# Kernel optimization log

Hardware: AMD Instinct MI355X
Metric: run time of the kernel (lower is better)

The kernel has to match this reference:

```python
import jax, jax.numpy as jnp
from jax import lax
import numpy as np

# Model hyper-parameters (from init_kwargs)
B = 4
POINT_NUM = 32768
SKP_NUM = 512
ISK_NUM = 2
K1 = 32                       # skp_neighbor_num
K2 = int(K1 * SKP_NUM * 4 / POINT_NUM)   # = 2, as computed in __init__
RADIUS_SCALING = 1.5
SPHERE_N = 128                # points per sphere template


def _fibonacci_sphere(n):
    i = np.arange(n, dtype=np.float64) + 0.5
    phi = np.arccos(1.0 - 2.0 * i / n)
    theta = np.pi * (1.0 + 5.0 ** 0.5) * i
    return np.stack([np.cos(theta) * np.sin(phi),
                     np.sin(theta) * np.sin(phi),
                     np.cos(phi)], axis=-1).astype(np.float32)


def setup_inputs() -> dict:
    key = jax.random.key(0)
    xyz = jax.random.normal(key, (B, POINT_NUM, 3), dtype=jnp.float32)
    sphere_template = jnp.asarray(_fibonacci_sphere(SPHERE_N))  # [S,3] unit sphere
    return {"xyz": xyz, "sphere_template": sphere_template}


def _fps(xyz, n):
    """Iterative furthest point sampling. xyz: [B,N,3] -> indices [B,n] int32."""
    b, N, _ = xyz.shape
    dist0 = jnp.full((b, N), 1e10, dtype=xyz.dtype)
    last0 = jnp.zeros((b,), dtype=jnp.int32)

    def step(carry, _):
        dist, last = carry
        lp = jnp.take_along_axis(xyz, last[:, None, None], axis=1)  # [B,1,3]
        d = jnp.sum((xyz - lp) ** 2, axis=-1)                        # [B,N]
        dist = jnp.minimum(dist, d)
        nxt = jnp.argmax(dist, axis=-1).astype(jnp.int32)
        return (dist, nxt), last

    (_, _), idxs = lax.scan(step, (dist0, last0), None, length=n)
    return idxs.T  # [B,n]


def _pairwise_sqdist(centers, pts):
    # [B,M,N] squared distances
    c2 = jnp.sum(centers ** 2, axis=-1)[:, :, None]
    p2 = jnp.sum(pts ** 2, axis=-1)[:, None, :]
    cp = jnp.einsum('bmd,bnd->bmn', centers, pts)
    return c2 + p2 - 2.0 * cp


def _sklnz(centers, pts, k):
    """SkeletonizationBlock: move each center to the mean of its k nearest
    points in pts; radius = mean distance to those neighbors."""
    d2 = _pairwise_sqdist(centers, pts)          # [B,M,N]
    neg, idx = lax.top_k(-d2, k)                 # [B,M,k]
    nb = jax.vmap(lambda x, i: x[i])(pts, idx)   # [B,M,k,3]
    new_centers = jnp.mean(nb, axis=2)
    radius = jnp.mean(jnp.sqrt(jnp.clip(-neg, 0.0)), axis=2)  # [B,M]
    return new_centers, radius


def _forward(xyz, sphere_template):
    # Stage 1: FPS to 4*skp_num seeds, then iterative skeletonization
    ids = _fps(xyz, SKP_NUM * 4)                               # [B,4*skp]
    centers = jnp.take_along_axis(xyz, ids[:, :, None], axis=1)
    radius = None
    for _ in range(ISK_NUM):
        centers, radius = _sklnz(centers, xyz, K1)
    # Stage 2: FPS on intermediate skeleton down to skp_num
    xyz2 = centers
    ids2 = _fps(xyz2, SKP_NUM)                                 # [B,skp]
    centers = jnp.take_along_axis(xyz2, ids2[:, :, None], axis=1)
    radius = jnp.take_along_axis(radius, ids2, axis=1)
    for _ in range(ISK_NUM):
        centers, _radius = _sklnz(centers, xyz2, K2)
    radius = (radius + _radius) * RADIUS_SCALING               # [B,skp]
    # Sphere reconstruction: template scaled by radius, translated to centers
    sphere_points = centers[:, :, None, :] + radius[:, :, None, None] * sphere_template[None, None]
    return centers, sphere_points, radius


def reference(xyz, sphere_template):
    return _forward(xyz, sphere_template)
```

## Files before the change

kernel.cpp:

```cpp
#include <hip/hip_runtime.h>
#include <cstdint>

#define BATCH 4
#define NPTS  32768
#define QN    8192
#define SKP   512
#define M1    (SKP*4)
#define KA    32
#define KB    2
#define SPHN  128

__device__ __forceinline__ float sqdist(float px, float py, float pz,
                                        float cx, float cy, float cz) {
  float dx = px - cx, dy = py - cy, dz = pz - cz;
  return __fadd_rn(__fadd_rn(__fmul_rn(dx, dx), __fmul_rn(dy, dy)),
                   __fmul_rn(dz, dz));
}
__device__ __forceinline__ float d2gram(float px, float py, float pz,
                                        float qx, float qy, float qz, float q2) {
  float p2 = __fadd_rn(__fadd_rn(__fmul_rn(px, px), __fmul_rn(py, py)),
                       __fmul_rn(pz, pz));
  float cp = __fadd_rn(__fadd_rn(__fmul_rn(qx, px), __fmul_rn(qy, py)),
                       __fmul_rn(qz, pz));
  return __fsub_rn(__fadd_rn(q2, p2), __fadd_rn(cp, cp));
}

__device__ __forceinline__ unsigned long long shfl_xor_u64(unsigned long long v, int off) {
  int lo = __shfl_xor((int)(unsigned)v, off);
  int hi = __shfl_xor((int)(unsigned)(v >> 32), off);
  return ((unsigned long long)(unsigned)hi << 32) | (unsigned)lo;
}
__device__ __forceinline__ unsigned long long shfl_u64(unsigned long long v, int src) {
  int lo = __shfl((int)(unsigned)v, src);
  int hi = __shfl((int)(unsigned)(v >> 32), src);
  return ((unsigned long long)(unsigned)hi << 32) | (unsigned)lo;
}
__device__ __forceinline__ unsigned long long umax64(unsigned long long a, unsigned long long b) {
  return a > b ? a : b;
}
__device__ __forceinline__ unsigned long long umin64(unsigned long long a, unsigned long long b) {
  return a < b ? a : b;
}
__device__ __forceinline__ void ins3(unsigned long long& k1, unsigned long long& k2,
                                     unsigned long long& k3, unsigned long long v) {
  k3 = umax64(k3, umin64(k2, v));
  k2 = umax64(k2, umin64(k1, v));
  k1 = umax64(k1, v);
}
__device__ __forceinline__ void ins4(unsigned long long& k1, unsigned long long& k2,
                                     unsigned long long& k3, unsigned long long& k4,
                                     unsigned long long v) {
  k4 = umax64(k4, umin64(k3, v));
  k3 = umax64(k3, umin64(k2, v));
  k2 = umax64(k2, umin64(k1, v));
  k1 = umax64(k1, v);
}

__global__ __launch_bounds__(1024)
void fps1_kernel(const float* __restrict__ xyz, float4* __restrict__ cen4a,
                 unsigned long long* __restrict__ sync)
{
  int blk = blockIdx.x;
  int b = blk >> 2, sub = blk & 3;
  const float* X = xyz + (size_t)b * NPTS * 3;
  cen4a += (size_t)b * M1;
  int tid = threadIdx.x, lane = tid & 63, wave = tid >> 6;
  int base = sub * QN;

  __shared__ float2 xysh[QN];
  __shared__ unsigned long long s_w[16][4];
  __shared__ float s_pivc[48][3];
  __shared__ int s_J;

  float zr[8], dist[8];
#pragma unroll
  for (int j = 0; j < 8; ++j) {
    int pl = tid + 1024 * j;
    int pg = base + pl;
    xysh[pl] = make_float2(X[3*pg], X[3*pg+1]);
    zr[j] = X[3*pg+2];
    dist[j] = 1e10f;
  }
  if (tid == 0) {
    s_pivc[0][0] = X[0]; s_pivc[0][1] = X[1]; s_pivc[0][2] = X[2];
    if (sub == 0) cen4a[0] = make_float4(X[0], X[1], X[2], 0.f);
  }
  __syncthreads();

  int it = 1, J = 1, rc = 1;

  while (it < M1) {
    for (int jp0 = 0; jp0 < J; jp0 += 4) {
      float pxa[4], pya[4], pza[4];
#pragma unroll
      for (int l = 0; l < 4; ++l) {
        int jj = jp0 + l; jj = (jj < J) ? jj : jp0;
        pxa[l] = s_pivc[jj][0]; pya[l] = s_pivc[jj][1]; pza[l] = s_pivc[jj][2];
      }
#pragma unroll
      for (int j = 0; j < 8; ++j) {
        int pl = tid + 1024 * j;
        float2 c2 = xysh[pl];
        float dd = dist[j];
#pragma unroll
        for (int l = 0; l < 4; ++l)
          dd = fminf(dd, sqdist(c2.x, c2.y, zr[j], pxa[l], pya[l], pza[l]));
        dist[j] = dd;
      }
    }
    unsigned long long k1 = 0, k2 = 0, k3 = 0, k4 = 0;
#pragma unroll
    for (int j = 0; j < 8; ++j) {
      int pg = base + tid + 1024 * j;
      unsigned long long key =
          ((unsigned long long)__float_as_uint(dist[j]) << 15) |
          (unsigned)(0x7FFF - pg);
      ins4(k1, k2, k3, k4, key);
    }
#pragma unroll
    for (int off = 32; off > 0; off >>= 1) {
      unsigned long long o1 = shfl_xor_u64(k1, off);
      unsigned long long o2 = shfl_xor_u64(k2, off);
      unsigned long long o3 = shfl_xor_u64(k3, off);
      unsigned long long o4 = shfl_xor_u64(k4, off);
      ins4(k1, k2, k3, k4, o1);
      ins4(k1, k2, k3, k4, o2);
      ins4(k1, k2, k3, k4, o3);
      ins4(k1, k2, k3, k4, o4);
    }
    if (lane == 0) {
      s_w[wave][0] = k1; s_w[wave][1] = k2; s_w[wave][2] = k3; s_w[wave][3] = k4;
    }
    __syncthreads();
    if (wave == 0) {
      unsigned long long fb = (lane < 16) ? s_w[lane][3] : 0;
#pragma unroll
      for (int off = 8; off > 0; off >>= 1) {
        unsigned long long o = shfl_xor_u64(fb, off);
        if (o > fb) fb = o;
      }
      fb = shfl_u64(fb, 0);
      unsigned tag = (unsigned)rc;
      int par = rc & 1;
      int sbase = ((b * 2 + par) * 4 + sub) * 56;
      if (lane < 48)
        __hip_atomic_store(&sync[sbase + lane],
                           (s_w[lane & 15][lane >> 4] << 12) | tag,
                           __ATOMIC_RELAXED, __HIP_MEMORY_SCOPE_AGENT);
      if (lane == 48)
        __hip_atomic_store(&sync[sbase + 48], (fb << 12) | tag,
                           __ATOMIC_RELAXED, __HIP_MEMORY_SCOPE_AGENT);
      unsigned long long ck[3];
      int slots[3]; bool need[3];
#pragma unroll
      for (int k = 0; k < 3; ++k) {
        int q = lane + 64 * k;
        int r = q / 48, s = q % 48;
        if (r == 0) { ck[k] = s_w[s & 15][s >> 4]; need[k] = false; slots[k] = 0; }
        else {
          slots[k] = ((b * 2 + par) * 4 + ((sub + r) & 3)) * 56 + s;
          need[k] = true; ck[k] = 0;
        }
      }
      bool needf = (lane < 3);
      int fslot = ((b * 2 + par) * 4 + ((sub + 1 + lane) & 3)) * 56 + 48;
      unsigned long long flr = 0;
      while (__any(need[0] || need[1] || need[2] || needf)) {
#pragma unroll
        for (int k = 0; k < 3; ++k) if (need[k]) {
          unsigned long long v = __hip_atomic_load(&sync[slots[k]],
                                  __ATOMIC_RELAXED, __HIP_MEMORY_SCOPE_AGENT);
          if ((unsigned)(v & 0xFFFu) == tag) { ck[k] = v >> 12; need[k] = false; }
        }
        if (needf) {
          unsigned long long v = __hip_atomic_load(&sync[fslot],
                                  __ATOMIC_RELAXED, __HIP_MEMORY_SCOPE_AGENT);
          if ((unsigned)(v & 0xFFFu) == tag) { flr = v >> 12; needf = false; }
        }
      }
      unsigned long long f = fb;
      f = umax64(f, shfl_u64(flr, 0));
      f = umax64(f, shfl_u64(flr, 1));
      f = umax64(f, shfl_u64(flr, 2));
      float cxx[3], cyy[3], czz[3];
#pragma unroll
      for (int k = 0; k < 3; ++k) {
        int ci = 0x7FFF - (int)(ck[k] & 0x7FFFu);
        cxx[k] = X[3*ci]; cyy[k] = X[3*ci+1]; czz[k] = X[3*ci+2];
      }
      int Jn = 0;
      while (it + Jn < M1 && Jn < 48) {
        unsigned long long mk = umax64(umax64(ck[0], ck[1]), ck[2]);
#pragma unroll
        for (int off = 32; off > 0; off >>= 1) {
          unsigned long long o = shfl_xor_u64(mk, off);
          if (o > mk) mk = o;
        }
        if (!(mk > f)) break;
        float px = 0.f, py = 0.f, pz = 0.f;
#pragma unroll
        for (int k = 0; k < 3; ++k) {
          unsigned long long bb = __ballot(ck[k] == mk);
          if (bb) {
            int wl = __ffsll((long long)bb) - 1;
            px = __shfl(cxx[k], wl); py = __shfl(cyy[k], wl); pz = __shfl(czz[k], wl);
            break;
          }
        }
        if (lane == 0) {
          s_pivc[Jn][0] = px; s_pivc[Jn][1] = py; s_pivc[Jn][2] = pz;
          if (sub == 0) cen4a[it + Jn] = make_float4(px, py, pz, 0.f);
        }
#pragma unroll
        for (int k = 0; k < 3; ++k) {
          float d = sqdist(cxx[k], cyy[k], czz[k], px, py, pz);
          float nv = fminf(__uint_as_float((unsigned)(ck[k] >> 15)), d);
          ck[k] = ((unsigned long long)__float_as_uint(nv) << 15) | (ck[k] & 0x7FFFu);
        }
        ++Jn;
      }
      if (lane == 0) s_J = Jn;
    }
    __syncthreads();
    J = s_J;
    it += J;
    rc += 1;
  }
}

__global__ __launch_bounds__(1024)
void fps2_kernel(const float4* __restrict__ pts, int* __restrict__ ids)
{
  int b = blockIdx.x;
  pts += (size_t)b * M1;
  ids += (size_t)b * SKP;
  int tid = threadIdx.x, lane = tid & 63, wave = tid >> 6;

  __shared__ float4 pl[M1];
  __shared__ unsigned long long s_w[16][3];
  __shared__ float s_pivc[16][3];
  __shared__ int s_J;

  float4 f0 = pts[tid], f1 = pts[tid + 1024];
  pl[tid] = f0; pl[tid + 1024] = f1;
  float dist0 = 1e10f, dist1 = 1e10f;
  if (tid == 0) {
    ids[0] = 0;
    s_pivc[0][0] = f0.x; s_pivc[0][1] = f0.y; s_pivc[0][2] = f0.z;
  }
  __syncthreads();

  int it = 1, J = 1;

  while (it < SKP) {
    for (int jp0 = 0; jp0 < J; jp0 += 4) {
      float pxa[4], pya[4], pza[4];
#pragma unroll
      for (int l = 0; l < 4; ++l) {
        int jj = jp0 + l; jj = (jj < J) ? jj : jp0;
        pxa[l] = s_pivc[jj][0]; pya[l] = s_pivc[jj][1]; pza[l] = s_pivc[jj][2];
      }
#pragma unroll
      for (int l = 0; l < 4; ++l) {
        dist0 = fminf(dist0, sqdist(f0.x, f0.y, f0.z, pxa[l], pya[l], pza[l]));
        dist1 = fminf(dist1, sqdist(f1.x, f1.y, f1.z, pxa[l], pya[l], pza[l]));
      }
    }
    unsigned long long k1, k2 = 0, k3 = 0;
    k1 = ((unsigned long long)__float_as_uint(dist0) << 15) | (unsigned)(0x7FFF - tid);
    {
      unsigned long long key =
          ((unsigned long long)__float_as_uint(dist1) << 15) | (unsigned)(0x7FFF - (tid + 1024));
      ins3(k1, k2, k3, key);
    }
#pragma unroll
    for (int off = 32; off > 0; off >>= 1) {
      unsigned long long o1 = shfl_xor_u64(k1, off);
      unsigned long long o2 = shfl_xor_u64(k2, off);
      unsigned long long o3 = shfl_xor_u64(k3, off);
      ins3(k1, k2, k3, o1);
      ins3(k1, k2, k3, o2);
      ins3(k1, k2, k3, o3);
    }
    if (lane == 0) { s_w[wave][0] = k1; s_w[wave][1] = k2; s_w[wave][2] = k3; }
    __syncthreads();
    if (wave == 0) {
      unsigned long long fb = (lane < 16) ? s_w[lane][2] : 0;
#pragma unroll
      for (int off = 8; off > 0; off >>= 1) {
        unsigned long long o = shfl_xor_u64(fb, off);
        if (o > fb) fb = o;
      }
      unsigned long long f = shfl_u64(fb, 0);
      unsigned long long ck = 0;
      if (lane < 16)      ck = s_w[lane][0];
      else if (lane < 32) ck = s_w[lane - 16][1];
      int ci = (0x7FFF - (int)(ck & 0x7FFFu)) & (M1 - 1);
      float4 c = pl[ci];
      int Jn = 0;
      while (it + Jn < SKP && Jn < 16) {
        unsigned long long mk = ck;
#pragma unroll
        for (int off = 32; off > 0; off >>= 1) {
          unsigned long long o = shfl_xor_u64(mk, off);
          if (o > mk) mk = o;
        }
        if (!(mk > f)) break;
        unsigned long long ball = __ballot(ck == mk);
        int wl = __ffsll((long long)ball) - 1;
        float px = __shfl(c.x, wl), py = __shfl(c.y, wl), pz = __shfl(c.z, wl);
        if (lane == 0) {
          s_pivc[Jn][0] = px; s_pivc[Jn][1] = py; s_pivc[Jn][2] = pz;
          ids[it + Jn] = 0x7FFF - (int)(mk & 0x7FFFu);
        }
        float d = sqdist(c.x, c.y, c.z, px, py, pz);
        float nv = fminf(__uint_as_float((unsigned)(ck >> 15)), d);
        ck = ((unsigned long long)__float_as_uint(nv) << 15) | (ck & 0x7FFFu);
        ++Jn;
      }
      if (lane == 0) s_J = Jn;
    }
    __syncthreads();
    J = s_J;
    it += J;
  }
}

template<int K, int KL, int N, bool S3>
__global__ __launch_bounds__(256)
void sklnz_kernel(const float4* __restrict__ queries,
                  const void*   __restrict__ ptsv,
                  float4* __restrict__ outc,
                  float*  __restrict__ outr,
                  int M)
{
  const int CH = N / 64;
  const int CHP = N / 256;
  int wave = threadIdx.x >> 6, lane = threadIdx.x & 63;
  int qid = blockIdx.x * 4 + wave;
  int b = qid / M;
  const float*  P3 = (const float*)ptsv + (size_t)b * N * 3;
  const float4* P4 = (const float4*)ptsv + (size_t)b * N;
  const float4* P4p = (const float4*)P3;
  float4 q = queries[qid];
  float q2 = __fadd_rn(__fadd_rn(__fmul_rn(q.x, q.x), __fmul_rn(q.y, q.y)),
                       __fmul_rn(q.z, q.z));

  __shared__ float heads[4][64][K + 1];

  float a[KL];
#pragma unroll
  for (int s = 0; s < KL; ++s) a[s] = 3.0e38f;
  if constexpr (S3) {
    for (int j = 0; j < CHP; ++j) {
      int u = lane + 64 * j;
      float4 A = P4p[3*u], B = P4p[3*u+1], C = P4p[3*u+2];
      float ds[4];
      ds[0] = d2gram(A.x, A.y, A.z, q.x, q.y, q.z, q2);
      ds[1] = d2gram(A.w, B.x, B.y, q.x, q.y, q.z, q2);
      ds[2] = d2gram(B.z, B.w, C.x, q.x, q.y, q.z, q2);
      ds[3] = d2gram(C.y, C.z, C.w, q.x, q.y, q.z, q2);
#pragma unroll
      for (int e = 0; e < 4; ++e) {
#pragma unroll
        for (int s = KL - 1; s > 0; --s) a[s] = fminf(a[s], fmaxf(a[s-1], ds[e]));
        a[0] = fminf(a[0], ds[e]);
      }
    }
  } else {
    for (int j = 0; j < CH; ++j) {
      float4 f = P4[lane + 64 * j];
      float d = d2gram(f.x, f.y, f.z, q.x, q.y, q.z, q2);
#pragma unroll
      for (int s = KL - 1; s > 0; --s) a[s] = fminf(a[s], fmaxf(a[s-1], d));
      a[0] = fminf(a[0], d);
    }
  }
#pragma unroll
  for (int s = 0; s < KL; ++s) heads[wave][lane][s] = a[s];
  heads[wave][lane][KL] = 3.1e38f;
  int h = 0; float t = 0.f;
  for (int r = 0; r < K; ++r) {
    float mv = heads[wave][lane][h];
    int   ml = lane;
#pragma unroll
    for (int off = 32; off > 0; off >>= 1) {
      float ov = __shfl_xor(mv, off);
      int   ol = __shfl_xor(ml, off);
      if (ov < mv || (ov == mv && ol < ml)) { mv = ov; ml = ol; }
    }
    t = mv;
    if (ml == lane) h++;
  }

  float sx = 0.f, sy = 0.f, sz = 0.f, sr = 0.f;
  int cl = 0;
  int myNext = 0x7fffffff;
  if constexpr (S3) {
    for (int j = 0; j < CHP; ++j) {
      int u = lane + 64 * j;
      float4 A = P4p[3*u], B = P4p[3*u+1], C = P4p[3*u+2];
      float pxs[4] = {A.x, A.w, B.z, C.y};
      float pys[4] = {A.y, B.x, B.w, C.z};
      float pzs[4] = {A.z, B.y, C.x, C.w};
#pragma unroll
      for (int e = 0; e < 4; ++e) {
        float d = d2gram(pxs[e], pys[e], pzs[e], q.x, q.y, q.z, q2);
        if (d < t) { sx += pxs[e]; sy += pys[e]; sz += pzs[e];
                     sr += sqrtf(fmaxf(d, 0.f)); cl++; }
        else if (d == t && myNext == 0x7fffffff) myNext = 4*u + e;
      }
    }
  } else {
    for (int j = 0; j < CH; ++j) {
      int p = lane + 64 * j;
      float4 f = P4[p];
      float d = d2gram(f.x, f.y, f.z, q.x, q.y, q.z, q2);
      if (d < t) { sx += f.x; sy += f.y; sz += f.z; sr += sqrtf(fmaxf(d, 0.f)); cl++; }
      else if (d == t && myNext == 0x7fffffff) myNext = p;
    }
  }
  int ctot = cl;
#pragma unroll
  for (int off = 32; off > 0; off >>= 1) ctot += __shfl_xor(ctot, off);

  if constexpr (KL < K) {
    if (ctot >= K) {
      float a2[K];
#pragma unroll
      for (int s = 0; s < K; ++s) a2[s] = 3.0e38f;
      for (int j = 0; j < CHP; ++j) {
        int u = lane + 64 * j;
        float4 A = P4p[3*u], B = P4p[3*u+1], C = P4p[3*u+2];
        float ds[4];
        ds[0] = d2gram(A.x, A.y, A.z, q.x, q.y, q.z, q2);
        ds[1] = d2gram(A.w, B.x, B.y, q.x, q.y, q.z, q2);
        ds[2] = d2gram(B.z, B.w, C.x, q.x, q.y, q.z, q2);
        ds[3] = d2gram(C.y, C.z, C.w, q.x, q.y, q.z, q2);
#pragma unroll
        for (int e = 0; e < 4; ++e) {
#pragma unroll
          for (int s = K - 1; s > 0; --s) a2[s] = fminf(a2[s], fmaxf(a2[s-1], ds[e]));
          a2[0] = fminf(a2[0], ds[e]);
        }
      }
#pragma unroll
      for (int s = 0; s < K; ++s) heads[wave][lane][s] = a2[s];
      heads[wave][lane][K] = 3.1e38f;
      h = 0;
      for (int r = 0; r < K; ++r) {
        float mv = heads[wave][lane][h];
        int   ml = lane;
#pragma unroll
        for (int off = 32; off > 0; off >>= 1) {
          float ov = __shfl_xor(mv, off);
          int   ol = __shfl_xor(ml, off);
          if (ov < mv || (ov == mv && ol < ml)) { mv = ov; ml = ol; }
        }
        t = mv;
        if (ml == lane) h++;
      }
      sx = sy = sz = sr = 0.f; cl = 0; myNext = 0x7fffffff;
      for (int j = 0; j < CHP; ++j) {
        int u = lane + 64 * j;
        float4 A = P4p[3*u], B = P4p[3*u+1], C = P4p[3*u+2];
        float pxs[4] = {A.x, A.w, B.z, C.y};
        float pys[4] = {A.y, B.x, B.w, C.z};
        float pzs[4] = {A.z, B.y, C.x, C.w};
#pragma unroll
        for (int e = 0; e < 4; ++e) {
          float d = d2gram(pxs[e], pys[e], pzs[e], q.x, q.y, q.z, q2);
          if (d < t) { sx += pxs[e]; sy += pys[e]; sz += pzs[e];
                       sr += sqrtf(fmaxf(d, 0.f)); cl++; }
          else if (d == t && myNext == 0x7fffffff) myNext = 4*u + e;
        }
      }
      ctot = cl;
#pragma unroll
      for (int off = 32; off > 0; off >>= 1) ctot += __shfl_xor(ctot, off);
    }
  }

  int need = K - ctot;
  float rt = sqrtf(fmaxf(t, 0.f));

  for (int e0 = 0; e0 < need; ++e0) {
    int mn = myNext;
#pragma unroll
    for (int off = 32; off > 0; off >>= 1) mn = min(mn, __shfl_xor(mn, off));
    if (myNext == mn) {
      float px, py, pz;
      if (S3) { px = P3[3*mn]; py = P3[3*mn+1]; pz = P3[3*mn+2]; }
      else    { float4 f = P4[mn]; px = f.x; py = f.y; pz = f.z; }
      sx += px; sy += py; sz += pz; sr += rt;
      int nx = 0x7fffffff;
      if constexpr (S3) {
        for (int j = ((mn >> 2) - lane) / 64; j < CHP && nx == 0x7fffffff; ++j) {
          int u = lane + 64 * j;
          float4 A = P4p[3*u], B = P4p[3*u+1], C = P4p[3*u+2];
          float pxs[4] = {A.x, A.w, B.z, C.y};
          float pys[4] = {A.y, B.x, B.w, C.z};
          float pzs[4] = {A.z, B.y, C.x, C.w};
#pragma unroll
          for (int e = 0; e < 4; ++e) {
            int p = 4*u + e;
            float d = d2gram(pxs[e], pys[e], pzs[e], q.x, q.y, q.z, q2);
            if (p > mn && d == t && nx == 0x7fffffff) nx = p;
          }
        }
      } else {
        for (int j = (mn - lane) / 64 + 1; j < CH && nx == 0x7fffffff; ++j) {
          int p = lane + 64 * j;
          float4 f = P4[p];
          float d = d2gram(f.x, f.y, f.z, q.x, q.y, q.z, q2);
          if (d == t) nx = p;
        }
      }
      myNext = nx;
    }
  }

#pragma unroll
  for (int off = 32; off > 0; off >>= 1) {
    sx += __shfl_xor(sx, off);
    sy += __shfl_xor(sy, off);
    sz += __shfl_xor(sz, off);
    sr += __shfl_xor(sr, off);
  }
  if (lane == 0) {
    const float inv = 1.0f / (float)K;
    outc[qid] = make_float4(sx * inv, sy * inv, sz * inv, 0.f);
    outr[qid] = sr * inv;
  }
}

__global__ void gather2_kernel(const float4* __restrict__ cen4,
                               const float* __restrict__ rad1,
                               const int* __restrict__ ids2,
                               float4* __restrict__ cen2,
                               float* __restrict__ radg)
{
  int g = blockIdx.x * 256 + threadIdx.x;
  if (g >= BATCH * SKP) return;
  int b = g / SKP;
  int p = ids2[g];
  cen2[g] = cen4[(size_t)b * M1 + p];
  radg[g] = rad1[(size_t)b * M1 + p];
}

__global__ void finalize_kernel(const float4* __restrict__ cen,
                                const float* __restrict__ radg,
                                const float* __restrict__ rad2,
                                const float* __restrict__ tmpl,
                                float* __restrict__ out)
{
  int g = blockIdx.x * 256 + threadIdx.x;
  int s = g >> 7;
  int j = g & 127;
  float4 c = cen[s];
  float r = __fmul_rn(__fadd_rn(radg[s], rad2[s]), 1.5f);
  float tx = tmpl[3*j], ty = tmpl[3*j+1], tz = tmpl[3*j+2];
  float* sp = out + BATCH * SKP * 3;
  sp[3*g]     = __fadd_rn(c.x, __fmul_rn(r, tx));
  sp[3*g + 1] = __fadd_rn(c.y, __fmul_rn(r, ty));
  sp[3*g + 2] = __fadd_rn(c.z, __fmul_rn(r, tz));
  if (j == 0) {
    out[3*s] = c.x; out[3*s+1] = c.y; out[3*s+2] = c.z;
    out[BATCH*SKP*3 + BATCH*SKP*SPHN*3 + s] = r;
  }
}

extern "C" void kernel_launch(void* const* d_in, const int* in_sizes, int n_in,
                              void* d_out, int out_size, void* d_ws, size_t ws_size,
                              hipStream_t stream)
{
  const float* xyz  = (const float*)d_in[0];
  const float* tmpl = (const float*)d_in[1];
  float* out = (float*)d_out;
  char* ws = (char*)d_ws;

  float4* cen4a = (float4*)(ws + 32768);
  float4* cen4b = (float4*)(ws + 163840);
  float*  rad1  = (float*) (ws + 294912);
  int*    ids2  = (int*)   (ws + 327680);
  float4* cen2a = (float4*)(ws + 335872);
  float4* cen2b = (float4*)(ws + 368640);
  float*  radg  = (float*) (ws + 401408);
  float*  rad2  = (float*) (ws + 409600);
  unsigned long long* sync = (unsigned long long*)(ws + 417792);

  fps1_kernel<<<BATCH * 4, 1024, 0, stream>>>(xyz, cen4a, sync);
  sklnz_kernel<KA, 4, NPTS, true><<<BATCH * M1 / 4, 256, 0, stream>>>(cen4a, xyz, cen4b, rad1, M1);
  sklnz_kernel<KA, 4, NPTS, true><<<BATCH * M1 / 4, 256, 0, stream>>>(cen4b, xyz, cen4a, rad1, M1);
  fps2_kernel<<<BATCH, 1024, 0, stream>>>(cen4a, ids2);
  gather2_kernel<<<(BATCH * SKP + 255) / 256, 256, 0, stream>>>(cen4a, rad1, ids2, cen2a, radg);
  sklnz_kernel<KB, KB, M1, false><<<BATCH * SKP / 4, 256, 0, stream>>>(cen2a, cen4a, cen2b, rad2, SKP);
  sklnz_kernel<KB, KB, M1, false><<<BATCH * SKP / 4, 256, 0, stream>>>(cen2b, cen4a, cen2a, rad2, SKP);
  finalize_kernel<<<BATCH * SKP * SPHN / 256, 256, 0, stream>>>(cen2a, radg, rad2, tmpl, out);
}
```

Measured before the change: 4.029 ms.

## Use per-wave top-8 bitonic candidate lists in batched FPS stage one

Each thread now sorts its 8 keys with a sorting network, and the wave merges top-8 lists through a bitonic butterfly instead of repeated top-4 insertion. The candidate set shared across the four cooperating blocks per batch grows from 48 to 112 keys per block, and coordinates are staged in shared memory. A larger pool should let more pivots be accepted per round before the 8th-largest floor is hit, cutting the number of cross-block sync rounds in the sequential FPS loop. In exchange there is more sync traffic and polling per round, plus more register and shared-memory use.

```diff
diff --git a/kernel.cpp b/kernel.cpp
--- a/kernel.cpp
+++ b/kernel.cpp
@@ -10,6 +10,8 @@
 #define KB    2
 #define SPHN  128
 
+typedef unsigned long long u64;
+
 __device__ __forceinline__ float sqdist(float px, float py, float pz,
                                         float cx, float cy, float cz) {
   float dx = px - cx, dy = py - cy, dz = pz - cz;
@@ -25,40 +27,27 @@
   return __fsub_rn(__fadd_rn(q2, p2), __fadd_rn(cp, cp));
 }
 
-__device__ __forceinline__ unsigned long long shfl_xor_u64(unsigned long long v, int off) {
+__device__ __forceinline__ u64 shfl_xor_u64(u64 v, int off) {
   int lo = __shfl_xor((int)(unsigned)v, off);
   int hi = __shfl_xor((int)(unsigned)(v >> 32), off);
-  return ((unsigned long long)(unsigned)hi << 32) | (unsigned)lo;
-}
-__device__ __forceinline__ unsigned long long shfl_u64(unsigned long long v, int src) {
+  return ((u64)(unsigned)hi << 32) | (unsigned)lo;
+}
+__device__ __forceinline__ u64 shfl_u64(u64 v, int src) {
   int lo = __shfl((int)(unsigned)v, src);
   int hi = __shfl((int)(unsigned)(v >> 32), src);
-  return ((unsigned long long)(unsigned)hi << 32) | (unsigned)lo;
-}
-__device__ __forceinline__ unsigned long long umax64(unsigned long long a, unsigned long long b) {
-  return a > b ? a : b;
-}
-__device__ __forceinline__ unsigned long long umin64(unsigned long long a, unsigned long long b) {
-  return a < b ? a : b;
-}
-__device__ __forceinline__ void ins3(unsigned long long& k1, unsigned long long& k2,
-                                     unsigned long long& k3, unsigned long long v) {
+  return ((u64)(unsigned)hi << 32) | (unsigned)lo;
+}
+__device__ __forceinline__ u64 umax64(u64 a, u64 b) { return a > b ? a : b; }
+__device__ __forceinline__ u64 umin64(u64 a, u64 b) { return a < b ? a : b; }
+__device__ __forceinline__ void ins3(u64& k1, u64& k2, u64& k3, u64 v) {
   k3 = umax64(k3, umin64(k2, v));
   k2 = umax64(k2, umin64(k1, v));
   k1 = umax64(k1, v);
 }
-__device__ __forceinline__ void ins4(unsigned long long& k1, unsigned long long& k2,
-                                     unsigned long long& k3, unsigned long long& k4,
-                                     unsigned long long v) {
-  k4 = umax64(k4, umin64(k3, v));
-  k3 = umax64(k3, umin64(k2, v));
-  k2 = umax64(k2, umin64(k1, v));
-  k1 = umax64(k1, v);
-}
 
 __global__ __launch_bounds__(1024)
 void fps1_kernel(const float* __restrict__ xyz, float4* __restrict__ cen4a,
-                 unsigned long long* __restrict__ sync)
+                 u64* __restrict__ sync)
 {
   int blk = blockIdx.x;
   int b = blk >> 2, sub = blk & 3;
@@ -68,7 +57,8 @@
   int base = sub * QN;
 
   __shared__ float2 xysh[QN];
-  __shared__ unsigned long long s_w[16][4];
+  __shared__ u64 s_w[16][8];
+  __shared__ float4 s_cc[448];
   __shared__ float s_pivc[48][3];
   __shared__ int s_J;
 
@@ -108,114 +98,121 @@
         dist[j] = dd;
       }
     }
-    unsigned long long k1 = 0, k2 = 0, k3 = 0, k4 = 0;
+    u64 kk[8];
 #pragma unroll
     for (int j = 0; j < 8; ++j) {
       int pg = base + tid + 1024 * j;
-      unsigned long long key =
-          ((unsigned long long)__float_as_uint(dist[j]) << 15) |
-          (unsigned)(0x7FFF - pg);
-      ins4(k1, k2, k3, k4, key);
-    }
-#pragma unroll
-    for (int off = 32; off > 0; off >>= 1) {
-      unsigned long long o1 = shfl_xor_u64(k1, off);
-      unsigned long long o2 = shfl_xor_u64(k2, off);
-      unsigned long long o3 = shfl_xor_u64(k3, off);
-      unsigned long long o4 = shfl_xor_u64(k4, off);
-      ins4(k1, k2, k3, k4, o1);
-      ins4(k1, k2, k3, k4, o2);
-      ins4(k1, k2, k3, k4, o3);
-      ins4(k1, k2, k3, k4, o4);
-    }
-    if (lane == 0) {
-      s_w[wave][0] = k1; s_w[wave][1] = k2; s_w[wave][2] = k3; s_w[wave][3] = k4;
+      kk[j] = ((u64)__float_as_uint(dist[j]) << 15) | (unsigned)(0x7FFF - pg);
+    }
+#define CE(A,B) { u64 _h = umax64(kk[A], kk[B]); kk[B] = umin64(kk[A], kk[B]); kk[A] = _h; }
+    CE(0,1) CE(2,3) CE(4,5) CE(6,7)
+    CE(0,2) CE(1,3) CE(4,6) CE(5,7)
+    CE(1,2) CE(5,6)
+    CE(0,4) CE(1,5) CE(2,6) CE(3,7)
+    CE(2,4) CE(3,5)
+    CE(1,2) CE(3,4) CE(5,6)
+#pragma unroll
+    for (int off = 1; off < 64; off <<= 1) {
+#pragma unroll
+      for (int i = 0; i < 4; ++i) {
+        u64 o_lo = shfl_xor_u64(kk[7-i], off);
+        u64 o_hi = shfl_xor_u64(kk[i], off);
+        u64 n_i  = umax64(kk[i], o_lo);
+        u64 n_7i = umax64(kk[7-i], o_hi);
+        kk[i] = n_i; kk[7-i] = n_7i;
+      }
+      CE(0,4) CE(1,5) CE(2,6) CE(3,7)
+      CE(0,2) CE(1,3) CE(4,6) CE(5,7)
+      CE(0,1) CE(2,3) CE(4,5) CE(6,7)
+    }
+#undef CE
+    unsigned tag = (unsigned)rc;
+    int par = rc & 1;
+    int sbase = ((b * 2 + par) * 4 + sub) * 128;
+    if (lane < 8) {
+      u64 kv = kk[0];
+      kv = (lane == 1) ? kk[1] : kv;
+      kv = (lane == 2) ? kk[2] : kv;
+      kv = (lane == 3) ? kk[3] : kv;
+      kv = (lane == 4) ? kk[4] : kv;
+      kv = (lane == 5) ? kk[5] : kv;
+      kv = (lane == 6) ? kk[6] : kv;
+      kv = (lane == 7) ? kk[7] : kv;
+      s_w[wave][lane] = kv;
+      int slot = (lane < 7) ? (sbase + lane * 16 + wave) : (sbase + 112 + wave);
+      __hip_atomic_store(&sync[slot], (kv << 12) | tag,
+                         __ATOMIC_RELAXED, __HIP_MEMORY_SCOPE_AGENT);
     }
     __syncthreads();
     if (wave == 0) {
-      unsigned long long fb = (lane < 16) ? s_w[lane][3] : 0;
-#pragma unroll
-      for (int off = 8; off > 0; off >>= 1) {
-        unsigned long long o = shfl_xor_u64(fb, off);
-        if (o > fb) fb = o;
-      }
-      fb = shfl_u64(fb, 0);
-      unsigned tag = (unsigned)rc;
-      int par = rc & 1;
-      int sbase = ((b * 2 + par) * 4 + sub) * 56;
-      if (lane < 48)
-        __hip_atomic_store(&sync[sbase + lane],
-                           (s_w[lane & 15][lane >> 4] << 12) | tag,
-                           __ATOMIC_RELAXED, __HIP_MEMORY_SCOPE_AGENT);
-      if (lane == 48)
-        __hip_atomic_store(&sync[sbase + 48], (fb << 12) | tag,
-                           __ATOMIC_RELAXED, __HIP_MEMORY_SCOPE_AGENT);
-      unsigned long long ck[3];
-      int slots[3]; bool need[3];
-#pragma unroll
-      for (int k = 0; k < 3; ++k) {
-        int q = lane + 64 * k;
-        int r = q / 48, s = q % 48;
-        if (r == 0) { ck[k] = s_w[s & 15][s >> 4]; need[k] = false; slots[k] = 0; }
-        else {
-          slots[k] = ((b * 2 + par) * 4 + ((sub + r) & 3)) * 56 + s;
-          need[k] = true; ck[k] = 0;
-        }
-      }
-      bool needf = (lane < 3);
-      int fslot = ((b * 2 + par) * 4 + ((sub + 1 + lane) & 3)) * 56 + 48;
-      unsigned long long flr = 0;
-      while (__any(need[0] || need[1] || need[2] || needf)) {
-#pragma unroll
-        for (int k = 0; k < 3; ++k) if (need[k]) {
-          unsigned long long v = __hip_atomic_load(&sync[slots[k]],
-                                  __ATOMIC_RELAXED, __HIP_MEMORY_SCOPE_AGENT);
-          if ((unsigned)(v & 0xFFFu) == tag) { ck[k] = v >> 12; need[k] = false; }
-        }
-        if (needf) {
-          unsigned long long v = __hip_atomic_load(&sync[fslot],
-                                  __ATOMIC_RELAXED, __HIP_MEMORY_SCOPE_AGENT);
-          if ((unsigned)(v & 0xFFFu) == tag) { flr = v >> 12; needf = false; }
-        }
-      }
-      unsigned long long f = fb;
-      f = umax64(f, shfl_u64(flr, 0));
-      f = umax64(f, shfl_u64(flr, 1));
-      f = umax64(f, shfl_u64(flr, 2));
-      float cxx[3], cyy[3], czz[3];
-#pragma unroll
-      for (int k = 0; k < 3; ++k) {
-        int ci = 0x7FFF - (int)(ck[k] & 0x7FFFu);
-        cxx[k] = X[3*ci]; cyy[k] = X[3*ci+1]; czz[k] = X[3*ci+2];
+      u64 fb = (lane < 16) ? s_w[lane][7] : 0;
+#pragma unroll
+      for (int off = 8; off > 0; off >>= 1) fb = umax64(fb, shfl_xor_u64(fb, off));
+      u64 f = shfl_u64(fb, 0);
+      u64 ck[8]; int pp[8];
+      ck[0] = s_w[lane & 15][lane >> 4];              pp[0] = lane;
+      ck[1] = (lane < 48) ? s_w[lane & 15][4 + (lane >> 4)] : 0;
+      pp[1] = (lane < 48) ? lane + 64 : -1;
+      int slots[6]; bool need[6]; int ss[6];
+#pragma unroll
+      for (int k = 0; k < 6; ++k) {
+        int m = lane + 64 * k;
+        int r = m >> 7, s = m & 127;
+        ss[k] = s;
+        int rblk = (sub + 1 + r) & 3;
+        slots[k] = ((b * 2 + par) * 4 + rblk) * 128 + s;
+        need[k] = true; ck[2 + k] = 0; pp[2 + k] = (s < 112) ? 112 * (r + 1) + s : -1;
+      }
+      for (;;) {
+        bool any = false;
+#pragma unroll
+        for (int k = 0; k < 6; ++k) if (need[k]) {
+          u64 v = __hip_atomic_load(&sync[slots[k]],
+                                    __ATOMIC_RELAXED, __HIP_MEMORY_SCOPE_AGENT);
+          if ((unsigned)(v & 0xFFFu) == tag) { ck[2 + k] = v >> 12; need[k] = false; }
+          else any = true;
+        }
+        if (!__any(any)) break;
+      }
+#pragma unroll
+      for (int k = 0; k < 6; ++k) {
+        if (ss[k] >= 112) { f = umax64(f, ck[2 + k]); ck[2 + k] = 0; }
+      }
+#pragma unroll
+      for (int off = 32; off > 0; off >>= 1) f = umax64(f, shfl_xor_u64(f, off));
+#pragma unroll
+      for (int k = 0; k < 8; ++k) {
+        if (pp[k] >= 0) {
+          int ci = 0x7FFF - (int)(ck[k] & 0x7FFFu);
+          s_cc[pp[k]] = make_float4(X[3*ci], X[3*ci+1], X[3*ci+2], 0.f);
+        }
       }
       int Jn = 0;
       while (it + Jn < M1 && Jn < 48) {
-        unsigned long long mk = umax64(umax64(ck[0], ck[1]), ck[2]);
-#pragma unroll
-        for (int off = 32; off > 0; off >>= 1) {
-          unsigned long long o = shfl_xor_u64(mk, off);
-          if (o > mk) mk = o;
-        }
+        u64 lmk = ck[0]; int li = 0;
+#pragma unroll
+        for (int k = 1; k < 8; ++k) if (ck[k] > lmk) { lmk = ck[k]; li = k; }
+        u64 mk = lmk;
+#pragma unroll
+        for (int off = 32; off > 0; off >>= 1) mk = umax64(mk, shfl_xor_u64(mk, off));
         if (!(mk > f)) break;
-        float px = 0.f, py = 0.f, pz = 0.f;
-#pragma unroll
-        for (int k = 0; k < 3; ++k) {
-          unsigned long long bb = __ballot(ck[k] == mk);
-          if (bb) {
-            int wl = __ffsll((long long)bb) - 1;
-            px = __shfl(cxx[k], wl); py = __shfl(cyy[k], wl); pz = __shfl(czz[k], wl);
-            break;
-          }
-        }
+        u64 ball = __ballot(lmk == mk);
+        int ow = __ffsll((long long)ball) - 1;
+        int lp = pp[0];
+#pragma unroll
+        for (int k = 1; k < 8; ++k) lp = (li == k) ? pp[k] : lp;
+        float4 c = s_cc[lp < 0 ? 0 : lp];
+        float px = __shfl(c.x, ow), py = __shfl(c.y, ow), pz = __shfl(c.z, ow);
         if (lane == 0) {
           s_pivc[Jn][0] = px; s_pivc[Jn][1] = py; s_pivc[Jn][2] = pz;
           if (sub == 0) cen4a[it + Jn] = make_float4(px, py, pz, 0.f);
         }
 #pragma unroll
-        for (int k = 0; k < 3; ++k) {
-          float d = sqdist(cxx[k], cyy[k], czz[k], px, py, pz);
+        for (int k = 0; k < 8; ++k) {
+          float4 cc = s_cc[pp[k] < 0 ? 0 : pp[k]];
+          float d = sqdist(cc.x, cc.y, cc.z, px, py, pz);
           float nv = fminf(__uint_as_float((unsigned)(ck[k] >> 15)), d);
-          ck[k] = ((unsigned long long)__float_as_uint(nv) << 15) | (ck[k] & 0x7FFFu);
+          ck[k] = ((u64)__float_as_uint(nv) << 15) | (ck[k] & 0x7FFFu);
         }
         ++Jn;
       }
@@ -237,7 +234,7 @@
   int tid = threadIdx.x, lane = tid & 63, wave = tid >> 6;
 
   __shared__ float4 pl[M1];
-  __shared__ unsigned long long s_w[16][3];
+  __shared__ u64 s_w[16][3];
   __shared__ float s_pivc[16][3];
   __shared__ int s_J;
 
@@ -266,18 +263,17 @@
         dist1 = fminf(dist1, sqdist(f1.x, f1.y, f1.z, pxa[l], pya[l], pza[l]));
       }
     }
-    unsigned long long k1, k2 = 0, k3 = 0;
-    k1 = ((unsigned long long)__float_as_uint(dist0) << 15) | (unsigned)(0x7FFF - tid);
+    u64 k1, k2 = 0, k3 = 0;
+    k1 = ((u64)__float_as_uint(dist0) << 15) | (unsigned)(0x7FFF - tid);
     {
-      unsigned long long key =
-          ((unsigned long long)__float_as_uint(dist1) << 15) | (unsigned)(0x7FFF - (tid + 1024));
+      u64 key = ((u64)__float_as_uint(dist1) << 15) | (unsigned)(0x7FFF - (tid + 1024));
       ins3(k1, k2, k3, key);
     }
 #pragma unroll
     for (int off = 32; off > 0; off >>= 1) {
-      unsigned long long o1 = shfl_xor_u64(k1, off);
-      unsigned long long o2 = shfl_xor_u64(k2, off);
-      unsigned long long o3 = shfl_xor_u64(k3, off);
+      u64 o1 = shfl_xor_u64(k1, off);
+      u64 o2 = shfl_xor_u64(k2, off);
+      u64 o3 = shfl_xor_u64(k3, off);
       ins3(k1, k2, k3, o1);
       ins3(k1, k2, k3, o2);
       ins3(k1, k2, k3, o3);
@@ -285,28 +281,28 @@
     if (lane == 0) { s_w[wave][0] = k1; s_w[wave][1] = k2; s_w[wave][2] = k3; }
     __syncthreads();
     if (wave == 0) {
-      unsigned long long fb = (lane < 16) ? s_w[lane][2] : 0;
+      u64 fb = (lane < 16) ? s_w[lane][2] : 0;
 #pragma unroll
       for (int off = 8; off > 0; off >>= 1) {
-        unsigned long long o = shfl_xor_u64(fb, off);
+        u64 o = shfl_xor_u64(fb, off);
         if (o > fb) fb = o;
       }
-      unsigned long long f = shfl_u64(fb, 0);
-      unsigned long long ck = 0;
+      u64 f = shfl_u64(fb, 0);
+      u64 ck = 0;
       if (lane < 16)      ck = s_w[lane][0];
       else if (lane < 32) ck = s_w[lane - 16][1];
       int ci = (0x7FFF - (int)(ck & 0x7FFFu)) & (M1 - 1);
       float4 c = pl[ci];
       int Jn = 0;
       while (it + Jn < SKP && Jn < 16) {
-        unsigned long long mk = ck;
+        u64 mk = ck;
 #pragma unroll
         for (int off = 32; off > 0; off >>= 1) {
-          unsigned long long o = shfl_xor_u64(mk, off);
+          u64 o = shfl_xor_u64(mk, off);
           if (o > mk) mk = o;
         }
         if (!(mk > f)) break;
-        unsigned long long ball = __ballot(ck == mk);
+        u64 ball = __ballot(ck == mk);
         int wl = __ffsll((long long)ball) - 1;
         float px = __shfl(c.x, wl), py = __shfl(c.y, wl), pz = __shfl(c.z, wl);
         if (lane == 0) {
@@ -315,7 +311,7 @@
         }
         float d = sqdist(c.x, c.y, c.z, px, py, pz);
         float nv = fminf(__uint_as_float((unsigned)(ck >> 15)), d);
-        ck = ((unsigned long long)__float_as_uint(nv) << 15) | (ck & 0x7FFFu);
+        ck = ((u64)__float_as_uint(nv) << 15) | (ck & 0x7FFFu);
         ++Jn;
       }
       if (lane == 0) s_J = Jn;
@@ -587,7 +583,7 @@
   float4* cen2b = (float4*)(ws + 368640);
   float*  radg  = (float*) (ws + 401408);
   float*  rad2  = (float*) (ws + 409600);
-  unsigned long long* sync = (unsigned long long*)(ws + 417792);
+  u64* sync = (u64*)(ws + 417792);
 
   fps1_kernel<<<BATCH * 4, 1024, 0, stream>>>(xyz, cen4a, sync);
   sklnz_kernel<KA, 4, NPTS, true><<<BATCH * M1 / 4, 256, 0, stream>>>(cen4a, xyz, cen4b, rad1, M1);
```

Measured after the change: 4.582 ms. 1.14x slower.
